# Kernel optimization log

Measured on AMD Instinct MI355X. Metric: run time of the kernel, lower is better.

## Reference

```python
import jax, jax.numpy as jnp
import numpy as np

D_MODEL, H, D_K, D_V = 512, 8, 64, 64
S_Q, S_KV = 2048, 2048


def setup_inputs() -> dict:
    key = jax.random.key(0)
    ks = jax.random.split(key, 11)
    sc = 0.02
    return {
        "embeddings": jax.random.normal(ks[0], (S_Q, D_MODEL), jnp.float32),
        "K": jax.random.normal(ks[1], (S_KV, D_MODEL), jnp.float32),
        "V": jax.random.normal(ks[2], (S_KV, D_MODEL), jnp.float32),
        # per-head projection weights (stacked over heads) + biases
        "Wq": jax.random.normal(ks[3], (H, D_MODEL, D_K), jnp.float32) * sc,
        "bq": jax.random.normal(ks[4], (H, D_K), jnp.float32) * sc,
        "Wk": jax.random.normal(ks[5], (H, D_MODEL, D_K), jnp.float32) * sc,
        "bk": jax.random.normal(ks[6], (H, D_K), jnp.float32) * sc,
        "Wv": jax.random.normal(ks[7], (H, D_MODEL, D_V), jnp.float32) * sc,
        "bv": jax.random.normal(ks[8], (H, D_V), jnp.float32) * sc,
        # final linear: [h*d_v -> d_model]
        "Wo": jax.random.normal(ks[9], (H * D_V, D_MODEL), jnp.float32) * sc,
        "bo": jax.random.normal(ks[10], (D_MODEL,), jnp.float32) * sc,
    }


def reference(embeddings, K, V, Wq, bq, Wk, bk, Wv, bv, Wo, bo):
    # Batched per-head projections (the original loops over h heads; math identical)
    q = jnp.einsum("sd,hdk->hsk", embeddings, Wq) + bq[:, None, :]  # [h, Sq, d_k]
    k = jnp.einsum("td,hdk->htk", K, Wk) + bk[:, None, :]           # [h, Skv, d_k]
    v = jnp.einsum("td,hdv->htv", V, Wv) + bv[:, None, :]           # [h, Skv, d_v]
    scores = jnp.einsum("hsk,htk->hst", q, k) / jnp.sqrt(jnp.asarray(D_K, q.dtype))
    attn = jax.nn.softmax(scores, axis=-1)                           # [h, Sq, Skv]
    out = jnp.einsum("hst,htv->hsv", attn, v)                        # [h, Sq, d_v]
    # torch.cat(results, dim=1): head 0's d_v columns first -> [Sq, h*d_v]
    concat = jnp.transpose(out, (1, 0, 2)).reshape(S_Q, H * D_V)
    return concat @ Wo + bo                                          # [Sq, d_model]
```

## Files before the change

kernel.cpp:

```cpp
#include <hip/hip_runtime.h>

#define SQ 2048
#define DM 512
#define NH 8
#define NSPLIT 4

typedef __bf16 bf16x8 __attribute__((ext_vector_type(8)));
typedef float f32x4 __attribute__((ext_vector_type(4)));
typedef unsigned short us8 __attribute__((ext_vector_type(8)));
typedef unsigned short us4 __attribute__((ext_vector_type(4)));

__device__ __forceinline__ unsigned short f2bf(float f) {
    unsigned u = __builtin_bit_cast(unsigned, f);
    u += 0x7fffu + ((u >> 16) & 1u);
    return (unsigned short)(u >> 16);
}
__device__ __forceinline__ float bf2f(unsigned short u) {
    return __builtin_bit_cast(float, (unsigned)u << 16);
}

__global__ __launch_bounds__(256) void convert_all(
    const float* __restrict__ emb, const float* __restrict__ Kin, const float* __restrict__ Vin,
    const float* __restrict__ Wq,  const float* __restrict__ Wk,  const float* __restrict__ Wv,
    const float* __restrict__ Wo,
    unsigned short* __restrict__ xe, unsigned short* __restrict__ xk, unsigned short* __restrict__ xv,
    unsigned short* __restrict__ Wt,
    unsigned short* __restrict__ Woth, unsigned short* __restrict__ Wotl)
{
    const int b = blockIdx.x, tid = threadIdx.x;
    __shared__ float ld[64 * 68];
    float4* ld4 = reinterpret_cast<float4*>(ld);

    if (b < 1536) {
        const int m = b >> 9;
        const float* src = (m == 0) ? emb : (m == 1) ? Kin : Vin;
        unsigned short* dst = (m == 0) ? xe : (m == 1) ? xk : xv;
        const int oct = (b & 511) * 256 + tid;
        const float4* s4 = reinterpret_cast<const float4*>(src + (size_t)oct * 8);
        float4 f0 = s4[0], f1 = s4[1];
        us8 o;
        o[0] = f2bf(f0.x); o[1] = f2bf(f0.y); o[2] = f2bf(f0.z); o[3] = f2bf(f0.w);
        o[4] = f2bf(f1.x); o[5] = f2bf(f1.y); o[6] = f2bf(f1.z); o[7] = f2bf(f1.w);
        *reinterpret_cast<us8*>(dst + (size_t)oct * 8) = o;
    } else if (b < 1728) {
        const int wi = b - 1536;
        const int idx = wi >> 3;
        const int kt = wi & 7;
        const int p = idx >> 3, h = idx & 7;
        const float* src = ((p == 0) ? Wq : (p == 1) ? Wk : Wv)
                         + (size_t)h * 512 * 64 + (size_t)kt * 64 * 64;
        unsigned short* dst = Wt + (size_t)idx * 64 * 512 + kt * 64;
        const int rr = tid >> 4, c4 = tid & 15;
        #pragma unroll
        for (int it = 0; it < 4; it++) {
            int r = rr + 16 * it;
            ld4[r * 17 + c4] = reinterpret_cast<const float4*>(src + (size_t)r * 64)[c4];
        }
        __syncthreads();
        #pragma unroll
        for (int it = 0; it < 2; it++) {
            int slot = tid + it * 256;
            int n = slot >> 3, g = slot & 7;
            us8 o;
            #pragma unroll
            for (int i = 0; i < 8; i++)
                o[i] = f2bf(ld[(g * 8 + i) * 68 + n]);
            *reinterpret_cast<us8*>(dst + (size_t)n * 512 + g * 8) = o;
        }
    } else {
        const int ti = b - 1728;
        const int kt = ti >> 3, nt = ti & 7;
        const float* src = Wo + (size_t)kt * 64 * 512 + nt * 64;
        const int rr = tid >> 4, c4 = tid & 15;
        #pragma unroll
        for (int it = 0; it < 4; it++) {
            int r = rr + 16 * it;
            ld4[r * 17 + c4] = reinterpret_cast<const float4*>(src + (size_t)r * 512)[c4];
        }
        __syncthreads();
        #pragma unroll
        for (int it = 0; it < 2; it++) {
            int slot = tid + it * 256;
            int n = slot >> 3, g = slot & 7;
            us8 oh, ol;
            #pragma unroll
            for (int i = 0; i < 8; i++) {
                float v = ld[(g * 8 + i) * 68 + n];
                unsigned short hi = f2bf(v);
                oh[i] = hi;
                ol[i] = f2bf(v - bf2f(hi));
            }
            size_t doff = (size_t)(nt * 64 + n) * 512 + kt * 64 + g * 8;
            *reinterpret_cast<us8*>(Woth + doff) = oh;
            *reinterpret_cast<us8*>(Wotl + doff) = ol;
        }
    }
}

__global__ __launch_bounds__(256) void qkv_mfma(
    const unsigned short* __restrict__ xe, const unsigned short* __restrict__ xk,
    const unsigned short* __restrict__ xv, const unsigned short* __restrict__ Wt,
    const float* __restrict__ bq, const float* __restrict__ bk, const float* __restrict__ bv,
    unsigned short* __restrict__ qo, unsigned short* __restrict__ ko, unsigned short* __restrict__ vo)
{
    const int p = blockIdx.z, h = blockIdx.y, s0 = blockIdx.x * 64;
    const unsigned short* X = (p == 0) ? xe : (p == 1) ? xk : xv;
    const unsigned short* W = Wt + (size_t)(p * 8 + h) * 64 * 512;
    const float* B = ((p == 0) ? bq : (p == 1) ? bk : bv) + h * 64;

    const int tid = threadIdx.x;
    const int w = tid >> 6, lane = tid & 63, cl = lane & 15, q4 = lane >> 4;
    const int sr = tid >> 3, sg = tid & 7;

    __shared__ unsigned short As[2][64 * 72];
    __shared__ unsigned short Bs[2][64 * 72];

    #pragma unroll
    for (int it = 0; it < 2; it++) {
        int r = sr + 32 * it;
        *reinterpret_cast<float4*>(&As[0][r * 72 + sg * 8]) =
            *reinterpret_cast<const float4*>(&X[(size_t)(s0 + r) * 512 + sg * 8]);
        *reinterpret_cast<float4*>(&Bs[0][r * 72 + sg * 8]) =
            *reinterpret_cast<const float4*>(&W[(size_t)r * 512 + sg * 8]);
    }

    f32x4 acc[4] = {};

    for (int c = 0; c < 8; c++) {
        __syncthreads();
        const int buf = c & 1;
        const bool more = (c + 1 < 8);
        float4 ar[2], br[2];
        if (more) {
            #pragma unroll
            for (int it = 0; it < 2; it++) {
                int r = sr + 32 * it;
                ar[it] = *reinterpret_cast<const float4*>(
                    &X[(size_t)(s0 + r) * 512 + (c + 1) * 64 + sg * 8]);
                br[it] = *reinterpret_cast<const float4*>(
                    &W[(size_t)r * 512 + (c + 1) * 64 + sg * 8]);
            }
        }

        bf16x8 a0 = *reinterpret_cast<const bf16x8*>(&As[buf][(16 * w + cl) * 72 + q4 * 8]);
        bf16x8 a1 = *reinterpret_cast<const bf16x8*>(&As[buf][(16 * w + cl) * 72 + 32 + q4 * 8]);
        #pragma unroll
        for (int nn = 0; nn < 4; nn++) {
            bf16x8 b0 = *reinterpret_cast<const bf16x8*>(&Bs[buf][(16 * nn + cl) * 72 + q4 * 8]);
            bf16x8 b1 = *reinterpret_cast<const bf16x8*>(&Bs[buf][(16 * nn + cl) * 72 + 32 + q4 * 8]);
            acc[nn] = __builtin_amdgcn_mfma_f32_16x16x32_bf16(a0, b0, acc[nn], 0, 0, 0);
            acc[nn] = __builtin_amdgcn_mfma_f32_16x16x32_bf16(a1, b1, acc[nn], 0, 0, 0);
        }

        if (more) {
            const int nbuf = buf ^ 1;
            #pragma unroll
            for (int it = 0; it < 2; it++) {
                int r = sr + 32 * it;
                *reinterpret_cast<float4*>(&As[nbuf][r * 72 + sg * 8]) = ar[it];
                *reinterpret_cast<float4*>(&Bs[nbuf][r * 72 + sg * 8]) = br[it];
            }
        }
    }

    if (p == 0) {
        const float QSCALE = 0.125f * 1.4426950408889634f;
        #pragma unroll
        for (int nn = 0; nn < 4; nn++) {
            int col = 16 * nn + cl;
            float bb = B[col];
            #pragma unroll
            for (int r = 0; r < 4; r++)
                qo[((size_t)h * SQ + s0 + 16 * w + q4 * 4 + r) * 64 + col] =
                    f2bf((acc[nn][r] + bb) * QSCALE);
        }
    } else if (p == 1) {
        #pragma unroll
        for (int nn = 0; nn < 4; nn++) {
            int col = 16 * nn + cl;
            float bb = B[col];
            #pragma unroll
            for (int r = 0; r < 4; r++)
                ko[((size_t)h * SQ + s0 + 16 * w + q4 * 4 + r) * 64 + col] =
                    f2bf(acc[nn][r] + bb);
        }
    } else {
        #pragma unroll
        for (int nn = 0; nn < 4; nn++) {
            int col = 16 * nn + cl;
            float bb = B[col];
            ushort4 o;
            o.x = f2bf(acc[nn][0] + bb);
            o.y = f2bf(acc[nn][1] + bb);
            o.z = f2bf(acc[nn][2] + bb);
            o.w = f2bf(acc[nn][3] + bb);
            *reinterpret_cast<ushort4*>(
                vo + ((size_t)h * 64 + col) * SQ + s0 + 16 * w + q4 * 4) = o;
        }
    }
}

#define PW 72

__global__ __launch_bounds__(256, 4) void attn_fwd(
    const unsigned short* __restrict__ qbf,
    const unsigned short* __restrict__ kbf,
    const unsigned short* __restrict__ vbf,
    float* __restrict__ Opart,
    float* __restrict__ lpart)
{
    const int h = blockIdx.y, s0 = blockIdx.x * 64, z = blockIdx.z;
    const int tid = threadIdx.x;
    const int w = tid >> 6, lane = tid & 63, cl = lane & 15, q4 = lane >> 4;
    const int NT = SQ / 64 / NSPLIT;
    const int t0 = z * NT;

    __shared__ unsigned short Ks[2][64 * PW];
    __shared__ unsigned short Vs[2][64 * PW];

    bf16x8 aq0 = *reinterpret_cast<const bf16x8*>(
        &qbf[((size_t)h * SQ + s0 + 16 * w + cl) * 64 + q4 * 8]);
    bf16x8 aq1 = *reinterpret_cast<const bf16x8*>(
        &qbf[((size_t)h * SQ + s0 + 16 * w + cl) * 64 + 32 + q4 * 8]);

    const int sr = tid >> 3, sg = tid & 7;
    const int kapA = 32 * (sg >> 2) + 16 * (sg & 1) + 4 * ((sg >> 1) & 1);

    #pragma unroll
    for (int it = 0; it < 2; it++) {
        int r = sr + 32 * it;
        *reinterpret_cast<float4*>(&Ks[0][r * PW + sg * 8]) =
            *reinterpret_cast<const float4*>(&kbf[((size_t)h * SQ + t0 * 64 + r) * 64 + sg * 8]);
        us8 vv = *reinterpret_cast<const us8*>(&vbf[((size_t)h * 64 + r) * SQ + t0 * 64 + sg * 8]);
        *reinterpret_cast<us4*>(&Vs[0][r * PW + kapA]) =
            __builtin_shufflevector(vv, vv, 0, 1, 2, 3);
        *reinterpret_cast<us4*>(&Vs[0][r * PW + kapA + 8]) =
            __builtin_shufflevector(vv, vv, 4, 5, 6, 7);
    }

    f32x4 o_acc[4] = {};
    float lsum = 0.f;

    for (int tl = 0; tl < NT; tl++) {
        __syncthreads();
        const int buf = tl & 1;
        const bool more = (tl + 1 < NT);
        float4 kr[2];
        us8 vr[2];
        if (more) {
            #pragma unroll
            for (int it = 0; it < 2; it++) {
                int r = sr + 32 * it;
                kr[it] = *reinterpret_cast<const float4*>(
                    &kbf[((size_t)h * SQ + (t0 + tl + 1) * 64 + r) * 64 + sg * 8]);
                vr[it] = *reinterpret_cast<const us8*>(
                    &vbf[((size_t)h * 64 + r) * SQ + (t0 + tl + 1) * 64 + sg * 8]);
            }
        }

        f32x4 s_acc[4] = {};
        #pragma unroll
        for (int nn = 0; nn < 4; nn++) {
            bf16x8 k0 = *reinterpret_cast<const bf16x8*>(&Ks[buf][(16 * nn + cl) * PW + q4 * 8]);
            bf16x8 k1 = *reinterpret_cast<const bf16x8*>(&Ks[buf][(16 * nn + cl) * PW + 32 + q4 * 8]);
            s_acc[nn] = __builtin_amdgcn_mfma_f32_16x16x32_bf16(k0, aq0, s_acc[nn], 0, 0, 0);
            s_acc[nn] = __builtin_amdgcn_mfma_f32_16x16x32_bf16(k1, aq1, s_acc[nn], 0, 0, 0);
        }

        bf16x8 ap0, ap1;
        #pragma unroll
        for (int nn = 0; nn < 4; nn++) {
            #pragma unroll
            for (int r = 0; r < 4; r++) {
                float pv = __builtin_amdgcn_exp2f(s_acc[nn][r]);
                lsum += pv;
                if (nn < 2) ap0[nn * 4 + r] = (__bf16)pv;
                else        ap1[(nn - 2) * 4 + r] = (__bf16)pv;
            }
        }

        #pragma unroll
        for (int nn = 0; nn < 4; nn++) {
            bf16x8 b0 = *reinterpret_cast<const bf16x8*>(&Vs[buf][(16 * nn + cl) * PW + q4 * 8]);
            bf16x8 b1 = *reinterpret_cast<const bf16x8*>(&Vs[buf][(16 * nn + cl) * PW + 32 + q4 * 8]);
            o_acc[nn] = __builtin_amdgcn_mfma_f32_16x16x32_bf16(ap0, b0, o_acc[nn], 0, 0, 0);
            o_acc[nn] = __builtin_amdgcn_mfma_f32_16x16x32_bf16(ap1, b1, o_acc[nn], 0, 0, 0);
        }

        if (more) {
            const int nbuf = buf ^ 1;
            #pragma unroll
            for (int it = 0; it < 2; it++) {
                int r = sr + 32 * it;
                *reinterpret_cast<float4*>(&Ks[nbuf][r * PW + sg * 8]) = kr[it];
                *reinterpret_cast<us4*>(&Vs[nbuf][r * PW + kapA]) =
                    __builtin_shufflevector(vr[it], vr[it], 0, 1, 2, 3);
                *reinterpret_cast<us4*>(&Vs[nbuf][r * PW + kapA + 8]) =
                    __builtin_shufflevector(vr[it], vr[it], 4, 5, 6, 7);
            }
        }
    }

    lsum += __shfl_xor(lsum, 16);
    lsum += __shfl_xor(lsum, 32);

    const size_t zb = (size_t)(z * NH + h);
    if (q4 == 0)
        lpart[zb * SQ + s0 + 16 * w + cl] = lsum;

    #pragma unroll
    for (int nn = 0; nn < 4; nn++)
        #pragma unroll
        for (int r = 0; r < 4; r++)
            Opart[(zb * SQ + s0 + 16 * w + q4 * 4 + r) * 64 + 16 * nn + cl] = o_acc[nn][r];
}

__global__ __launch_bounds__(256) void attn_combine(
    const float* __restrict__ Opart, const float* __restrict__ lpart,
    unsigned short* __restrict__ athi, unsigned short* __restrict__ atlo)
{
    const int gid = blockIdx.x * 256 + threadIdx.x;
    const int s = gid >> 6, oct = gid & 63;
    const int col0 = oct * 8, h = col0 >> 6, dv0 = col0 & 63;

    float l = 0.f;
    #pragma unroll
    for (int z = 0; z < NSPLIT; z++)
        l += lpart[(size_t)(z * NH + h) * SQ + s];
    const float inv = 1.0f / l;

    float o[8] = {};
    #pragma unroll
    for (int z = 0; z < NSPLIT; z++) {
        const float4* base = reinterpret_cast<const float4*>(
            Opart + ((size_t)(z * NH + h) * SQ + s) * 64 + dv0);
        float4 a = base[0], bq = base[1];
        o[0] += a.x; o[1] += a.y; o[2] += a.z; o[3] += a.w;
        o[4] += bq.x; o[5] += bq.y; o[6] += bq.z; o[7] += bq.w;
    }
    us8 hi, lo;
    #pragma unroll
    for (int i = 0; i < 8; i++) {
        float v = o[i] * inv;
        unsigned short hb = f2bf(v);
        hi[i] = hb;
        lo[i] = f2bf(v - bf2f(hb));
    }
    *reinterpret_cast<us8*>(athi + (size_t)s * DM + col0) = hi;
    *reinterpret_cast<us8*>(atlo + (size_t)s * DM + col0) = lo;
}

__global__ __launch_bounds__(256) void out_proj(
    const unsigned short* __restrict__ ah, const unsigned short* __restrict__ al,
    const unsigned short* __restrict__ Wh, const unsigned short* __restrict__ Wl,
    const float* __restrict__ bo, float* __restrict__ out)
{
    const int s0 = blockIdx.x * 64, n0 = blockIdx.y * 64;
    const int tid = threadIdx.x;
    const int w = tid >> 6, lane = tid & 63, cl = lane & 15, q4 = lane >> 4;
    const int sr = tid >> 3, sg = tid & 7;

    __shared__ unsigned short Ah[2][64 * 72], Al[2][64 * 72];
    __shared__ unsigned short Bh[2][64 * 72], Bl[2][64 * 72];

    #pragma unroll
    for (int it = 0; it < 2; it++) {
        int r = sr + 32 * it;
        *reinterpret_cast<float4*>(&Ah[0][r * 72 + sg * 8]) =
            *reinterpret_cast<const float4*>(&ah[(size_t)(s0 + r) * 512 + sg * 8]);
        *reinterpret_cast<float4*>(&Al[0][r * 72 + sg * 8]) =
            *reinterpret_cast<const float4*>(&al[(size_t)(s0 + r) * 512 + sg * 8]);
        *reinterpret_cast<float4*>(&Bh[0][r * 72 + sg * 8]) =
            *reinterpret_cast<const float4*>(&Wh[(size_t)(n0 + r) * 512 + sg * 8]);
        *reinterpret_cast<float4*>(&Bl[0][r * 72 + sg * 8]) =
            *reinterpret_cast<const float4*>(&Wl[(size_t)(n0 + r) * 512 + sg * 8]);
    }

    f32x4 acc[4] = {};

    for (int c = 0; c < 8; c++) {
        __syncthreads();
        const int buf = c & 1;
        const bool more = (c + 1 < 8);
        float4 ahr[2], alr[2], bhr[2], blr[2];
        if (more) {
            #pragma unroll
            for (int it = 0; it < 2; it++) {
                int r = sr + 32 * it;
                int off = (c + 1) * 64 + sg * 8;
                ahr[it] = *reinterpret_cast<const float4*>(&ah[(size_t)(s0 + r) * 512 + off]);
                alr[it] = *reinterpret_cast<const float4*>(&al[(size_t)(s0 + r) * 512 + off]);
                bhr[it] = *reinterpret_cast<const float4*>(&Wh[(size_t)(n0 + r) * 512 + off]);
                blr[it] = *reinterpret_cast<const float4*>(&Wl[(size_t)(n0 + r) * 512 + off]);
            }
        }

        bf16x8 ah0 = *reinterpret_cast<const bf16x8*>(&Ah[buf][(16 * w + cl) * 72 + q4 * 8]);
        bf16x8 ah1 = *reinterpret_cast<const bf16x8*>(&Ah[buf][(16 * w + cl) * 72 + 32 + q4 * 8]);
        bf16x8 al0 = *reinterpret_cast<const bf16x8*>(&Al[buf][(16 * w + cl) * 72 + q4 * 8]);
        bf16x8 al1 = *reinterpret_cast<const bf16x8*>(&Al[buf][(16 * w + cl) * 72 + 32 + q4 * 8]);
        #pragma unroll
        for (int nn = 0; nn < 4; nn++) {
            bf16x8 bh0 = *reinterpret_cast<const bf16x8*>(&Bh[buf][(16 * nn + cl) * 72 + q4 * 8]);
            bf16x8 bh1 = *reinterpret_cast<const bf16x8*>(&Bh[buf][(16 * nn + cl) * 72 + 32 + q4 * 8]);
            bf16x8 bl0 = *reinterpret_cast<const bf16x8*>(&Bl[buf][(16 * nn + cl) * 72 + q4 * 8]);
            bf16x8 bl1 = *reinterpret_cast<const bf16x8*>(&Bl[buf][(16 * nn + cl) * 72 + 32 + q4 * 8]);
            acc[nn] = __builtin_amdgcn_mfma_f32_16x16x32_bf16(ah0, bh0, acc[nn], 0, 0, 0);
            acc[nn] = __builtin_amdgcn_mfma_f32_16x16x32_bf16(ah1, bh1, acc[nn], 0, 0, 0);
            acc[nn] = __builtin_amdgcn_mfma_f32_16x16x32_bf16(ah0, bl0, acc[nn], 0, 0, 0);
            acc[nn] = __builtin_amdgcn_mfma_f32_16x16x32_bf16(ah1, bl1, acc[nn], 0, 0, 0);
            acc[nn] = __builtin_amdgcn_mfma_f32_16x16x32_bf16(al0, bh0, acc[nn], 0, 0, 0);
            acc[nn] = __builtin_amdgcn_mfma_f32_16x16x32_bf16(al1, bh1, acc[nn], 0, 0, 0);
        }

        if (more) {
            const int nbuf = buf ^ 1;
            #pragma unroll
            for (int it = 0; it < 2; it++) {
                int r = sr + 32 * it;
                *reinterpret_cast<float4*>(&Ah[nbuf][r * 72 + sg * 8]) = ahr[it];
                *reinterpret_cast<float4*>(&Al[nbuf][r * 72 + sg * 8]) = alr[it];
                *reinterpret_cast<float4*>(&Bh[nbuf][r * 72 + sg * 8]) = bhr[it];
                *reinterpret_cast<float4*>(&Bl[nbuf][r * 72 + sg * 8]) = blr[it];
            }
        }
    }

    #pragma unroll
    for (int nn = 0; nn < 4; nn++) {
        int col = n0 + 16 * nn + cl;
        float bb = bo[col];
        #pragma unroll
        for (int r = 0; r < 4; r++)
            out[(size_t)(s0 + 16 * w + q4 * 4 + r) * DM + col] = acc[nn][r] + bb;
    }
}

extern "C" void kernel_launch(void* const* d_in, const int* in_sizes, int n_in,
                              void* d_out, int out_size, void* d_ws, size_t ws_size,
                              hipStream_t stream) {
    const float* emb = (const float*)d_in[0];
    const float* Kin = (const float*)d_in[1];
    const float* Vin = (const float*)d_in[2];
    const float* Wq  = (const float*)d_in[3];
    const float* bq  = (const float*)d_in[4];
    const float* Wk  = (const float*)d_in[5];
    const float* bk  = (const float*)d_in[6];
    const float* Wv  = (const float*)d_in[7];
    const float* bv  = (const float*)d_in[8];
    const float* Wo  = (const float*)d_in[9];
    const float* bo  = (const float*)d_in[10];
    float* out = (float*)d_out;

    unsigned short* p = (unsigned short*)d_ws;
    unsigned short* xe   = p; p += (size_t)SQ * DM;
    unsigned short* xk   = p; p += (size_t)SQ * DM;
    unsigned short* xv   = p; p += (size_t)SQ * DM;
    unsigned short* Wt   = p; p += (size_t)24 * 64 * 512;
    unsigned short* Woth = p; p += (size_t)512 * 512;
    unsigned short* Wotl = p; p += (size_t)512 * 512;
    unsigned short* qbf  = p; p += (size_t)NH * SQ * 64;
    unsigned short* kbf  = p; p += (size_t)NH * SQ * 64;
    unsigned short* vbf  = p; p += (size_t)NH * SQ * 64;
    unsigned short* athi = p; p += (size_t)SQ * DM;
    unsigned short* atlo = p; p += (size_t)SQ * DM;
    float* Opart = (float*)p;
    float* lpart = Opart + (size_t)NSPLIT * NH * SQ * 64;

    convert_all<<<1792, 256, 0, stream>>>(emb, Kin, Vin, Wq, Wk, Wv, Wo,
                                          xe, xk, xv, Wt, Woth, Wotl);
    qkv_mfma<<<dim3(32, 8, 3), 256, 0, stream>>>(xe, xk, xv, Wt, bq, bk, bv,
                                                 qbf, kbf, vbf);
    attn_fwd<<<dim3(32, 8, NSPLIT), 256, 0, stream>>>(qbf, kbf, vbf, Opart, lpart);
    attn_combine<<<512, 256, 0, stream>>>(Opart, lpart, athi, atlo);
    out_proj<<<dim3(32, 8), 256, 0, stream>>>(athi, atlo, Woth, Wotl, bo, out);
}
```

Measured before the change: 121.2 us.

## Process two query sub-tiles per wave in attention to reuse K/V tiles

Each attention block now covers 128 query rows instead of 64, with each wave handling two 16-row query sub-tiles that share the same K and V fragments loaded from shared memory. This halves the number of blocks and the global/LDS traffic for K/V per query row, and gives more MFMA work per LDS read. In exchange it doubles the accumulator registers, lowers the occupancy hint to 2, and halves the grid to 512 blocks, which may underfill the GPU.

Result: no change. 122.3 us (+0.9%).

```diff
diff --git a/kernel.cpp b/kernel.cpp
--- a/kernel.cpp
+++ b/kernel.cpp
@@ -202,14 +202,14 @@
 
 #define PW 72
 
-__global__ __launch_bounds__(256, 4) void attn_fwd(
+__global__ __launch_bounds__(256, 2) void attn_fwd(
     const unsigned short* __restrict__ qbf,
     const unsigned short* __restrict__ kbf,
     const unsigned short* __restrict__ vbf,
     float* __restrict__ Opart,
     float* __restrict__ lpart)
 {
-    const int h = blockIdx.y, s0 = blockIdx.x * 64, z = blockIdx.z;
+    const int h = blockIdx.y, s0 = blockIdx.x * 128, z = blockIdx.z;
     const int tid = threadIdx.x;
     const int w = tid >> 6, lane = tid & 63, cl = lane & 15, q4 = lane >> 4;
     const int NT = SQ / 64 / NSPLIT;
@@ -218,10 +218,15 @@
     __shared__ unsigned short Ks[2][64 * PW];
     __shared__ unsigned short Vs[2][64 * PW];
 
-    bf16x8 aq0 = *reinterpret_cast<const bf16x8*>(
-        &qbf[((size_t)h * SQ + s0 + 16 * w + cl) * 64 + q4 * 8]);
-    bf16x8 aq1 = *reinterpret_cast<const bf16x8*>(
-        &qbf[((size_t)h * SQ + s0 + 16 * w + cl) * 64 + 32 + q4 * 8]);
+    const size_t qbase = (size_t)h * SQ + s0 + 32 * w;
+    bf16x8 aq[2][2];
+    #pragma unroll
+    for (int qs = 0; qs < 2; qs++) {
+        aq[qs][0] = *reinterpret_cast<const bf16x8*>(
+            &qbf[(qbase + 16 * qs + cl) * 64 + q4 * 8]);
+        aq[qs][1] = *reinterpret_cast<const bf16x8*>(
+            &qbf[(qbase + 16 * qs + cl) * 64 + 32 + q4 * 8]);
+    }
 
     const int sr = tid >> 3, sg = tid & 7;
     const int kapA = 32 * (sg >> 2) + 16 * (sg & 1) + 4 * ((sg >> 1) & 1);
@@ -238,8 +243,8 @@
             __builtin_shufflevector(vv, vv, 4, 5, 6, 7);
     }
 
-    f32x4 o_acc[4] = {};
-    float lsum = 0.f;
+    f32x4 o_acc[2][4] = {};
+    float lsum[2] = {};
 
     for (int tl = 0; tl < NT; tl++) {
         __syncthreads();
@@ -258,24 +263,29 @@
             }
         }
 
-        f32x4 s_acc[4] = {};
+        f32x4 s_acc[2][4] = {};
         #pragma unroll
         for (int nn = 0; nn < 4; nn++) {
             bf16x8 k0 = *reinterpret_cast<const bf16x8*>(&Ks[buf][(16 * nn + cl) * PW + q4 * 8]);
             bf16x8 k1 = *reinterpret_cast<const bf16x8*>(&Ks[buf][(16 * nn + cl) * PW + 32 + q4 * 8]);
-            s_acc[nn] = __builtin_amdgcn_mfma_f32_16x16x32_bf16(k0, aq0, s_acc[nn], 0, 0, 0);
-            s_acc[nn] = __builtin_amdgcn_mfma_f32_16x16x32_bf16(k1, aq1, s_acc[nn], 0, 0, 0);
-        }
-
-        bf16x8 ap0, ap1;
-        #pragma unroll
-        for (int nn = 0; nn < 4; nn++) {
-            #pragma unroll
-            for (int r = 0; r < 4; r++) {
-                float pv = __builtin_amdgcn_exp2f(s_acc[nn][r]);
-                lsum += pv;
-                if (nn < 2) ap0[nn * 4 + r] = (__bf16)pv;
-                else        ap1[(nn - 2) * 4 + r] = (__bf16)pv;
+            #pragma unroll
+            for (int qs = 0; qs < 2; qs++) {
+                s_acc[qs][nn] = __builtin_amdgcn_mfma_f32_16x16x32_bf16(k0, aq[qs][0], s_acc[qs][nn], 0, 0, 0);
+                s_acc[qs][nn] = __builtin_amdgcn_mfma_f32_16x16x32_bf16(k1, aq[qs][1], s_acc[qs][nn], 0, 0, 0);
+            }
+        }
+
+        bf16x8 ap[2][2];
+        #pragma unroll
+        for (int qs = 0; qs < 2; qs++) {
+            #pragma unroll
+            for (int nn = 0; nn < 4; nn++) {
+                #pragma unroll
+                for (int r = 0; r < 4; r++) {
+                    float pv = __builtin_amdgcn_exp2f(s_acc[qs][nn][r]);
+                    lsum[qs] += pv;
+                    ap[qs][nn >> 1][(nn & 1) * 4 + r] = (__bf16)pv;
+                }
             }
         }
 
@@ -283,8 +293,11 @@
         for (int nn = 0; nn < 4; nn++) {
             bf16x8 b0 = *reinterpret_cast<const bf16x8*>(&Vs[buf][(16 * nn + cl) * PW + q4 * 8]);
             bf16x8 b1 = *reinterpret_cast<const bf16x8*>(&Vs[buf][(16 * nn + cl) * PW + 32 + q4 * 8]);
-            o_acc[nn] = __builtin_amdgcn_mfma_f32_16x16x32_bf16(ap0, b0, o_acc[nn], 0, 0, 0);
-            o_acc[nn] = __builtin_amdgcn_mfma_f32_16x16x32_bf16(ap1, b1, o_acc[nn], 0, 0, 0);
+            #pragma unroll
+            for (int qs = 0; qs < 2; qs++) {
+                o_acc[qs][nn] = __builtin_amdgcn_mfma_f32_16x16x32_bf16(ap[qs][0], b0, o_acc[qs][nn], 0, 0, 0);
+                o_acc[qs][nn] = __builtin_amdgcn_mfma_f32_16x16x32_bf16(ap[qs][1], b1, o_acc[qs][nn], 0, 0, 0);
+            }
         }
 
         if (more) {
@@ -301,18 +314,25 @@
         }
     }
 
-    lsum += __shfl_xor(lsum, 16);
-    lsum += __shfl_xor(lsum, 32);
-
     const size_t zb = (size_t)(z * NH + h);
-    if (q4 == 0)
-        lpart[zb * SQ + s0 + 16 * w + cl] = lsum;
-
-    #pragma unroll
-    for (int nn = 0; nn < 4; nn++)
-        #pragma unroll
-        for (int r = 0; r < 4; r++)
-            Opart[(zb * SQ + s0 + 16 * w + q4 * 4 + r) * 64 + 16 * nn + cl] = o_acc[nn][r];
+
+    #pragma unroll
+    for (int qs = 0; qs < 2; qs++) {
+        float v = lsum[qs];
+        v += __shfl_xor(v, 16);
+        v += __shfl_xor(v, 32);
+        if (q4 == 0)
+            lpart[zb * SQ + s0 + 32 * w + 16 * qs + cl] = v;
+    }
+
+    #pragma unroll
+    for (int qs = 0; qs < 2; qs++)
+        #pragma unroll
+        for (int nn = 0; nn < 4; nn++)
+            #pragma unroll
+            for (int r = 0; r < 4; r++)
+                Opart[(zb * SQ + s0 + 32 * w + 16 * qs + q4 * 4 + r) * 64 + 16 * nn + cl] =
+                    o_acc[qs][nn][r];
 }
 
 __global__ __launch_bounds__(256) void attn_combine(
@@ -471,7 +491,7 @@
                                           xe, xk, xv, Wt, Woth, Wotl);
     qkv_mfma<<<dim3(32, 8, 3), 256, 0, stream>>>(xe, xk, xv, Wt, bq, bk, bv,
                                                  qbf, kbf, vbf);
-    attn_fwd<<<dim3(32, 8, NSPLIT), 256, 0, stream>>>(qbf, kbf, vbf, Opart, lpart);
+    attn_fwd<<<dim3(16, 8, NSPLIT), 256, 0, stream>>>(qbf, kbf, vbf, Opart, lpart);
     attn_combine<<<512, 256, 0, stream>>>(Opart, lpart, athi, atlo);
     out_proj<<<dim3(32, 8), 256, 0, stream>>>(athi, atlo, Woth, Wotl, bo, out);
 }
```

## Restructure attention: per-wave KV tiles in registers, LDS tree reduction, fewer splits

Applied to the files above, without the earlier changes.

The attention kernel now uses 512-thread blocks, and each wave owns a distinct 64-key tile that it loads straight from global memory into registers, with no shared-memory staging or double buffering. Each wave covers all four 16-row query slabs, and the eight waves' partial outputs are summed through a shared-memory tree reduction. Row sums are computed with an MFMA against a ones vector instead of scalar adds, the split count drops from 4 to 2, and block IDs are swizzled across XCDs. This trades the per-tile syncs and LDS traffic for more register pressure, a larger LDS reduction buffer, and less parallelism across KV splits.

Result: slower. 170.2 us (+40.4%).

```diff
diff --git a/kernel.cpp b/kernel.cpp
--- a/kernel.cpp
+++ b/kernel.cpp
@@ -3,7 +3,7 @@
 #define SQ 2048
 #define DM 512
 #define NH 8
-#define NSPLIT 4
+#define NSPLIT 2
 
 typedef __bf16 bf16x8 __attribute__((ext_vector_type(8)));
 typedef float f32x4 __attribute__((ext_vector_type(4)));
@@ -200,119 +200,143 @@
     }
 }
 
-#define PW 72
-
-__global__ __launch_bounds__(256, 4) void attn_fwd(
+__global__ __launch_bounds__(512, 4) void attn_fwd(
     const unsigned short* __restrict__ qbf,
     const unsigned short* __restrict__ kbf,
     const unsigned short* __restrict__ vbf,
     float* __restrict__ Opart,
     float* __restrict__ lpart)
 {
-    const int h = blockIdx.y, s0 = blockIdx.x * 64, z = blockIdx.z;
+    const int bid = (blockIdx.x & 7) * 64 + (blockIdx.x >> 3);
+    const int x = bid & 31, h = (bid >> 5) & 7, z = bid >> 8;
+    const int s0 = x * 64;
     const int tid = threadIdx.x;
     const int w = tid >> 6, lane = tid & 63, cl = lane & 15, q4 = lane >> 4;
-    const int NT = SQ / 64 / NSPLIT;
-    const int t0 = z * NT;
-
-    __shared__ unsigned short Ks[2][64 * PW];
-    __shared__ unsigned short Vs[2][64 * PW];
-
-    bf16x8 aq0 = *reinterpret_cast<const bf16x8*>(
-        &qbf[((size_t)h * SQ + s0 + 16 * w + cl) * 64 + q4 * 8]);
-    bf16x8 aq1 = *reinterpret_cast<const bf16x8*>(
-        &qbf[((size_t)h * SQ + s0 + 16 * w + cl) * 64 + 32 + q4 * 8]);
-
-    const int sr = tid >> 3, sg = tid & 7;
-    const int kapA = 32 * (sg >> 2) + 16 * (sg & 1) + 4 * ((sg >> 1) & 1);
-
-    #pragma unroll
-    for (int it = 0; it < 2; it++) {
-        int r = sr + 32 * it;
-        *reinterpret_cast<float4*>(&Ks[0][r * PW + sg * 8]) =
-            *reinterpret_cast<const float4*>(&kbf[((size_t)h * SQ + t0 * 64 + r) * 64 + sg * 8]);
-        us8 vv = *reinterpret_cast<const us8*>(&vbf[((size_t)h * 64 + r) * SQ + t0 * 64 + sg * 8]);
-        *reinterpret_cast<us4*>(&Vs[0][r * PW + kapA]) =
-            __builtin_shufflevector(vv, vv, 0, 1, 2, 3);
-        *reinterpret_cast<us4*>(&Vs[0][r * PW + kapA + 8]) =
-            __builtin_shufflevector(vv, vv, 4, 5, 6, 7);
-    }
-
-    f32x4 o_acc[4] = {};
-    float lsum = 0.f;
-
-    for (int tl = 0; tl < NT; tl++) {
-        __syncthreads();
-        const int buf = tl & 1;
-        const bool more = (tl + 1 < NT);
-        float4 kr[2];
-        us8 vr[2];
-        if (more) {
-            #pragma unroll
-            for (int it = 0; it < 2; it++) {
-                int r = sr + 32 * it;
-                kr[it] = *reinterpret_cast<const float4*>(
-                    &kbf[((size_t)h * SQ + (t0 + tl + 1) * 64 + r) * 64 + sg * 8]);
-                vr[it] = *reinterpret_cast<const us8*>(
-                    &vbf[((size_t)h * 64 + r) * SQ + (t0 + tl + 1) * 64 + sg * 8]);
-            }
-        }
-
-        f32x4 s_acc[4] = {};
-        #pragma unroll
-        for (int nn = 0; nn < 4; nn++) {
-            bf16x8 k0 = *reinterpret_cast<const bf16x8*>(&Ks[buf][(16 * nn + cl) * PW + q4 * 8]);
-            bf16x8 k1 = *reinterpret_cast<const bf16x8*>(&Ks[buf][(16 * nn + cl) * PW + 32 + q4 * 8]);
-            s_acc[nn] = __builtin_amdgcn_mfma_f32_16x16x32_bf16(k0, aq0, s_acc[nn], 0, 0, 0);
-            s_acc[nn] = __builtin_amdgcn_mfma_f32_16x16x32_bf16(k1, aq1, s_acc[nn], 0, 0, 0);
-        }
-
-        bf16x8 ap0, ap1;
-        #pragma unroll
-        for (int nn = 0; nn < 4; nn++) {
-            #pragma unroll
-            for (int r = 0; r < 4; r++) {
-                float pv = __builtin_amdgcn_exp2f(s_acc[nn][r]);
-                lsum += pv;
-                if (nn < 2) ap0[nn * 4 + r] = (__bf16)pv;
-                else        ap1[(nn - 2) * 4 + r] = (__bf16)pv;
-            }
-        }
-
-        #pragma unroll
-        for (int nn = 0; nn < 4; nn++) {
-            bf16x8 b0 = *reinterpret_cast<const bf16x8*>(&Vs[buf][(16 * nn + cl) * PW + q4 * 8]);
-            bf16x8 b1 = *reinterpret_cast<const bf16x8*>(&Vs[buf][(16 * nn + cl) * PW + 32 + q4 * 8]);
-            o_acc[nn] = __builtin_amdgcn_mfma_f32_16x16x32_bf16(ap0, b0, o_acc[nn], 0, 0, 0);
-            o_acc[nn] = __builtin_amdgcn_mfma_f32_16x16x32_bf16(ap1, b1, o_acc[nn], 0, 0, 0);
-        }
-
-        if (more) {
-            const int nbuf = buf ^ 1;
-            #pragma unroll
-            for (int it = 0; it < 2; it++) {
-                int r = sr + 32 * it;
-                *reinterpret_cast<float4*>(&Ks[nbuf][r * PW + sg * 8]) = kr[it];
-                *reinterpret_cast<us4*>(&Vs[nbuf][r * PW + kapA]) =
-                    __builtin_shufflevector(vr[it], vr[it], 0, 1, 2, 3);
-                *reinterpret_cast<us4*>(&Vs[nbuf][r * PW + kapA + 8]) =
-                    __builtin_shufflevector(vr[it], vr[it], 4, 5, 6, 7);
-            }
-        }
-    }
-
-    lsum += __shfl_xor(lsum, 16);
-    lsum += __shfl_xor(lsum, 32);
+
+    __shared__ float Obuf[4][65 * 68];
+
+    bf16x8 aq[4][2];
+    #pragma unroll
+    for (int qs = 0; qs < 4; qs++) {
+        const unsigned short* qb = &qbf[((size_t)h * SQ + s0 + 16 * qs + cl) * 64 + q4 * 8];
+        aq[qs][0] = *reinterpret_cast<const bf16x8*>(qb);
+        aq[qs][1] = *reinterpret_cast<const bf16x8*>(qb + 32);
+    }
+
+    bf16x8 vone;
+    #pragma unroll
+    for (int i = 0; i < 8; i++) vone[i] = (__bf16)1.0f;
+
+    f32x4 o_acc[4][4] = {};
+    f32x4 l_acc[4] = {};
+
+    #pragma unroll
+    for (int ti = 0; ti < 2; ti++) {
+        const int tg = (z * 16 + ti * 8 + w) * 64;
+
+        const unsigned short* kb = &kbf[((size_t)h * SQ + tg + cl) * 64 + q4 * 8];
+        bf16x8 kf[4][2];
+        #pragma unroll
+        for (int nn = 0; nn < 4; nn++) {
+            kf[nn][0] = *reinterpret_cast<const bf16x8*>(kb + nn * 1024);
+            kf[nn][1] = *reinterpret_cast<const bf16x8*>(kb + nn * 1024 + 32);
+        }
+
+        bf16x8 bb[4][2];
+        #pragma unroll
+        for (int nn = 0; nn < 4; nn++) {
+            const unsigned short* vb =
+                &vbf[((size_t)(h * 64 + 16 * nn + cl)) * SQ + tg + q4 * 4];
+            us4 v0 = *reinterpret_cast<const us4*>(vb);
+            us4 v1 = *reinterpret_cast<const us4*>(vb + 16);
+            us4 v2 = *reinterpret_cast<const us4*>(vb + 32);
+            us4 v3 = *reinterpret_cast<const us4*>(vb + 48);
+            bb[nn][0] = __builtin_bit_cast(bf16x8,
+                __builtin_shufflevector(v0, v1, 0, 1, 2, 3, 4, 5, 6, 7));
+            bb[nn][1] = __builtin_bit_cast(bf16x8,
+                __builtin_shufflevector(v2, v3, 0, 1, 2, 3, 4, 5, 6, 7));
+        }
+
+        #pragma unroll
+        for (int qs = 0; qs < 4; qs++) {
+            f32x4 s[4] = {};
+            #pragma unroll
+            for (int nn = 0; nn < 4; nn++) {
+                s[nn] = __builtin_amdgcn_mfma_f32_16x16x32_bf16(kf[nn][0], aq[qs][0], s[nn], 0, 0, 0);
+                s[nn] = __builtin_amdgcn_mfma_f32_16x16x32_bf16(kf[nn][1], aq[qs][1], s[nn], 0, 0, 0);
+            }
+
+            bf16x8 ap0, ap1;
+            #pragma unroll
+            for (int nn = 0; nn < 4; nn++)
+                #pragma unroll
+                for (int r = 0; r < 4; r++) {
+                    float pv = __builtin_amdgcn_exp2f(s[nn][r]);
+                    if (nn < 2) ap0[nn * 4 + r] = (__bf16)pv;
+                    else        ap1[(nn - 2) * 4 + r] = (__bf16)pv;
+                }
+
+            l_acc[qs] = __builtin_amdgcn_mfma_f32_16x16x32_bf16(ap0, vone, l_acc[qs], 0, 0, 0);
+            l_acc[qs] = __builtin_amdgcn_mfma_f32_16x16x32_bf16(ap1, vone, l_acc[qs], 0, 0, 0);
+
+            #pragma unroll
+            for (int nn = 0; nn < 4; nn++) {
+                o_acc[qs][nn] = __builtin_amdgcn_mfma_f32_16x16x32_bf16(ap0, bb[nn][0], o_acc[qs][nn], 0, 0, 0);
+                o_acc[qs][nn] = __builtin_amdgcn_mfma_f32_16x16x32_bf16(ap1, bb[nn][1], o_acc[qs][nn], 0, 0, 0);
+            }
+        }
+    }
+
+    auto write_partial = [&](int b) {
+        #pragma unroll
+        for (int qs = 0; qs < 4; qs++) {
+            #pragma unroll
+            for (int nn = 0; nn < 4; nn++)
+                *reinterpret_cast<f32x4*>(&Obuf[b][(16 * nn + cl) * 68 + 16 * qs + 4 * q4]) =
+                    o_acc[qs][nn];
+            if (cl == 0)
+                *reinterpret_cast<f32x4*>(&Obuf[b][64 * 68 + 16 * qs + 4 * q4]) = l_acc[qs];
+        }
+    };
+    auto add_partial = [&](int b) {
+        #pragma unroll
+        for (int qs = 0; qs < 4; qs++) {
+            #pragma unroll
+            for (int nn = 0; nn < 4; nn++)
+                o_acc[qs][nn] += *reinterpret_cast<const f32x4*>(
+                    &Obuf[b][(16 * nn + cl) * 68 + 16 * qs + 4 * q4]);
+            l_acc[qs] += *reinterpret_cast<const f32x4*>(
+                &Obuf[b][64 * 68 + 16 * qs + 4 * q4]);
+        }
+    };
+
+    if (w >= 4) write_partial(w - 4);
+    __syncthreads();
+    if (w < 4) add_partial(w);
+    __syncthreads();
+    if (w == 2 || w == 3) write_partial(w - 2);
+    __syncthreads();
+    if (w < 2) add_partial(w);
+    __syncthreads();
+    if (w == 1) write_partial(0);
+    __syncthreads();
+    if (w == 0) { add_partial(0); write_partial(0); }
+    __syncthreads();
 
     const size_t zb = (size_t)(z * NH + h);
-    if (q4 == 0)
-        lpart[zb * SQ + s0 + 16 * w + cl] = lsum;
-
-    #pragma unroll
-    for (int nn = 0; nn < 4; nn++)
-        #pragma unroll
-        for (int r = 0; r < 4; r++)
-            Opart[(zb * SQ + s0 + 16 * w + q4 * 4 + r) * 64 + 16 * nn + cl] = o_acc[nn][r];
+    #pragma unroll
+    for (int i = 0; i < 2; i++) {
+        int c = i * 512 + tid;
+        int q = c >> 4, d4 = c & 15;
+        float4 o;
+        o.x = Obuf[0][(d4 * 4 + 0) * 68 + q];
+        o.y = Obuf[0][(d4 * 4 + 1) * 68 + q];
+        o.z = Obuf[0][(d4 * 4 + 2) * 68 + q];
+        o.w = Obuf[0][(d4 * 4 + 3) * 68 + q];
+        *reinterpret_cast<float4*>(&Opart[(zb * SQ + s0 + q) * 64 + d4 * 4]) = o;
+    }
+    if (tid < 64)
+        lpart[zb * SQ + s0 + tid] = Obuf[0][64 * 68 + tid];
 }
 
 __global__ __launch_bounds__(256) void attn_combine(
@@ -471,7 +495,7 @@
                                           xe, xk, xv, Wt, Woth, Wotl);
     qkv_mfma<<<dim3(32, 8, 3), 256, 0, stream>>>(xe, xk, xv, Wt, bq, bk, bv,
                                                  qbf, kbf, vbf);
-    attn_fwd<<<dim3(32, 8, NSPLIT), 256, 0, stream>>>(qbf, kbf, vbf, Opart, lpart);
+    attn_fwd<<<512, 512, 0, stream>>>(qbf, kbf, vbf, Opart, lpart);
     attn_combine<<<512, 256, 0, stream>>>(Opart, lpart, athi, atlo);
     out_proj<<<dim3(32, 8), 256, 0, stream>>>(athi, atlo, Woth, Wotl, bo, out);
 }
```

## Halve out_proj row tile and load A fragments directly from global memory

Applied to the files above, without the earlier changes.

The output projection now uses 32-row tiles instead of 64, which doubles the grid to 512 blocks to fill more CUs. It also drops the LDS staging for the activation hi/lo operands: each wave reads its A fragments straight from global memory while only the weight tiles stay double-buffered in shared memory. Waves are now split across output columns rather than rows. This cuts LDS usage and traffic and raises occupancy, at the cost of uncoalesced, redundant global reads of A across waves and more total weight reloads.

New measurement: 130.9 us. +8.0%, slower.

```diff
diff --git a/kernel.cpp b/kernel.cpp
--- a/kernel.cpp
+++ b/kernel.cpp
@@ -350,67 +350,68 @@
     *reinterpret_cast<us8*>(atlo + (size_t)s * DM + col0) = lo;
 }
 
-__global__ __launch_bounds__(256) void out_proj(
+__global__ __launch_bounds__(256, 4) void out_proj(
     const unsigned short* __restrict__ ah, const unsigned short* __restrict__ al,
     const unsigned short* __restrict__ Wh, const unsigned short* __restrict__ Wl,
     const float* __restrict__ bo, float* __restrict__ out)
 {
-    const int s0 = blockIdx.x * 64, n0 = blockIdx.y * 64;
+    const int s0 = blockIdx.x * 32, n0 = blockIdx.y * 64;
     const int tid = threadIdx.x;
     const int w = tid >> 6, lane = tid & 63, cl = lane & 15, q4 = lane >> 4;
     const int sr = tid >> 3, sg = tid & 7;
 
-    __shared__ unsigned short Ah[2][64 * 72], Al[2][64 * 72];
     __shared__ unsigned short Bh[2][64 * 72], Bl[2][64 * 72];
 
     #pragma unroll
     for (int it = 0; it < 2; it++) {
         int r = sr + 32 * it;
-        *reinterpret_cast<float4*>(&Ah[0][r * 72 + sg * 8]) =
-            *reinterpret_cast<const float4*>(&ah[(size_t)(s0 + r) * 512 + sg * 8]);
-        *reinterpret_cast<float4*>(&Al[0][r * 72 + sg * 8]) =
-            *reinterpret_cast<const float4*>(&al[(size_t)(s0 + r) * 512 + sg * 8]);
         *reinterpret_cast<float4*>(&Bh[0][r * 72 + sg * 8]) =
             *reinterpret_cast<const float4*>(&Wh[(size_t)(n0 + r) * 512 + sg * 8]);
         *reinterpret_cast<float4*>(&Bl[0][r * 72 + sg * 8]) =
             *reinterpret_cast<const float4*>(&Wl[(size_t)(n0 + r) * 512 + sg * 8]);
     }
 
-    f32x4 acc[4] = {};
+    f32x4 acc[2] = {};
 
     for (int c = 0; c < 8; c++) {
         __syncthreads();
         const int buf = c & 1;
         const bool more = (c + 1 < 8);
-        float4 ahr[2], alr[2], bhr[2], blr[2];
+        float4 bhr[2], blr[2];
         if (more) {
             #pragma unroll
             for (int it = 0; it < 2; it++) {
                 int r = sr + 32 * it;
                 int off = (c + 1) * 64 + sg * 8;
-                ahr[it] = *reinterpret_cast<const float4*>(&ah[(size_t)(s0 + r) * 512 + off]);
-                alr[it] = *reinterpret_cast<const float4*>(&al[(size_t)(s0 + r) * 512 + off]);
                 bhr[it] = *reinterpret_cast<const float4*>(&Wh[(size_t)(n0 + r) * 512 + off]);
                 blr[it] = *reinterpret_cast<const float4*>(&Wl[(size_t)(n0 + r) * 512 + off]);
             }
         }
 
-        bf16x8 ah0 = *reinterpret_cast<const bf16x8*>(&Ah[buf][(16 * w + cl) * 72 + q4 * 8]);
-        bf16x8 ah1 = *reinterpret_cast<const bf16x8*>(&Ah[buf][(16 * w + cl) * 72 + 32 + q4 * 8]);
-        bf16x8 al0 = *reinterpret_cast<const bf16x8*>(&Al[buf][(16 * w + cl) * 72 + q4 * 8]);
-        bf16x8 al1 = *reinterpret_cast<const bf16x8*>(&Al[buf][(16 * w + cl) * 72 + 32 + q4 * 8]);
-        #pragma unroll
-        for (int nn = 0; nn < 4; nn++) {
-            bf16x8 bh0 = *reinterpret_cast<const bf16x8*>(&Bh[buf][(16 * nn + cl) * 72 + q4 * 8]);
-            bf16x8 bh1 = *reinterpret_cast<const bf16x8*>(&Bh[buf][(16 * nn + cl) * 72 + 32 + q4 * 8]);
-            bf16x8 bl0 = *reinterpret_cast<const bf16x8*>(&Bl[buf][(16 * nn + cl) * 72 + q4 * 8]);
-            bf16x8 bl1 = *reinterpret_cast<const bf16x8*>(&Bl[buf][(16 * nn + cl) * 72 + 32 + q4 * 8]);
-            acc[nn] = __builtin_amdgcn_mfma_f32_16x16x32_bf16(ah0, bh0, acc[nn], 0, 0, 0);
-            acc[nn] = __builtin_amdgcn_mfma_f32_16x16x32_bf16(ah1, bh1, acc[nn], 0, 0, 0);
-            acc[nn] = __builtin_amdgcn_mfma_f32_16x16x32_bf16(ah0, bl0, acc[nn], 0, 0, 0);
-            acc[nn] = __builtin_amdgcn_mfma_f32_16x16x32_bf16(ah1, bl1, acc[nn], 0, 0, 0);
-            acc[nn] = __builtin_amdgcn_mfma_f32_16x16x32_bf16(al0, bh0, acc[nn], 0, 0, 0);
-            acc[nn] = __builtin_amdgcn_mfma_f32_16x16x32_bf16(al1, bh1, acc[nn], 0, 0, 0);
+        bf16x8 ahf[2][2], alf[2][2];
+        #pragma unroll
+        for (int ms = 0; ms < 2; ms++) {
+            const unsigned short* abh = &ah[(size_t)(s0 + 16 * ms + cl) * 512 + c * 64 + q4 * 8];
+            const unsigned short* abl = &al[(size_t)(s0 + 16 * ms + cl) * 512 + c * 64 + q4 * 8];
+            ahf[ms][0] = *reinterpret_cast<const bf16x8*>(abh);
+            ahf[ms][1] = *reinterpret_cast<const bf16x8*>(abh + 32);
+            alf[ms][0] = *reinterpret_cast<const bf16x8*>(abl);
+            alf[ms][1] = *reinterpret_cast<const bf16x8*>(abl + 32);
+        }
+
+        bf16x8 bh0 = *reinterpret_cast<const bf16x8*>(&Bh[buf][(16 * w + cl) * 72 + q4 * 8]);
+        bf16x8 bh1 = *reinterpret_cast<const bf16x8*>(&Bh[buf][(16 * w + cl) * 72 + 32 + q4 * 8]);
+        bf16x8 bl0 = *reinterpret_cast<const bf16x8*>(&Bl[buf][(16 * w + cl) * 72 + q4 * 8]);
+        bf16x8 bl1 = *reinterpret_cast<const bf16x8*>(&Bl[buf][(16 * w + cl) * 72 + 32 + q4 * 8]);
+
+        #pragma unroll
+        for (int ms = 0; ms < 2; ms++) {
+            acc[ms] = __builtin_amdgcn_mfma_f32_16x16x32_bf16(ahf[ms][0], bh0, acc[ms], 0, 0, 0);
+            acc[ms] = __builtin_amdgcn_mfma_f32_16x16x32_bf16(ahf[ms][1], bh1, acc[ms], 0, 0, 0);
+            acc[ms] = __builtin_amdgcn_mfma_f32_16x16x32_bf16(ahf[ms][0], bl0, acc[ms], 0, 0, 0);
+            acc[ms] = __builtin_amdgcn_mfma_f32_16x16x32_bf16(ahf[ms][1], bl1, acc[ms], 0, 0, 0);
+            acc[ms] = __builtin_amdgcn_mfma_f32_16x16x32_bf16(alf[ms][0], bh0, acc[ms], 0, 0, 0);
+            acc[ms] = __builtin_amdgcn_mfma_f32_16x16x32_bf16(alf[ms][1], bh1, acc[ms], 0, 0, 0);
         }
 
         if (more) {
@@ -418,22 +419,19 @@
             #pragma unroll
             for (int it = 0; it < 2; it++) {
                 int r = sr + 32 * it;
-                *reinterpret_cast<float4*>(&Ah[nbuf][r * 72 + sg * 8]) = ahr[it];
-                *reinterpret_cast<float4*>(&Al[nbuf][r * 72 + sg * 8]) = alr[it];
                 *reinterpret_cast<float4*>(&Bh[nbuf][r * 72 + sg * 8]) = bhr[it];
                 *reinterpret_cast<float4*>(&Bl[nbuf][r * 72 + sg * 8]) = blr[it];
             }
         }
     }
 
-    #pragma unroll
-    for (int nn = 0; nn < 4; nn++) {
-        int col = n0 + 16 * nn + cl;
-        float bb = bo[col];
+    const int col = n0 + 16 * w + cl;
+    const float bb = bo[col];
+    #pragma unroll
+    for (int ms = 0; ms < 2; ms++)
         #pragma unroll
         for (int r = 0; r < 4; r++)
-            out[(size_t)(s0 + 16 * w + q4 * 4 + r) * DM + col] = acc[nn][r] + bb;
-    }
+            out[(size_t)(s0 + 16 * ms + q4 * 4 + r) * DM + col] = acc[ms][r] + bb;
 }
 
 extern "C" void kernel_launch(void* const* d_in, const int* in_sizes, int n_in,
@@ -473,5 +471,5 @@
                                                  qbf, kbf, vbf);
     attn_fwd<<<dim3(32, 8, NSPLIT), 256, 0, stream>>>(qbf, kbf, vbf, Opart, lpart);
     attn_combine<<<512, 256, 0, stream>>>(Opart, lpart, athi, atlo);
-    out_proj<<<dim3(32, 8), 256, 0, stream>>>(athi, atlo, Woth, Wotl, bo, out);
-}
+    out_proj<<<dim3(64, 8), 256, 0, stream>>>(athi, atlo, Woth, Wotl, bo, out);
+}
```
